# Kernel optimization log

Measured on AMD Instinct MI355X. Metric: run time of the kernel, lower is better.

## Reference

```python
import jax, jax.numpy as jnp
import numpy as np

N, C, T, V = 64, 256, 64, 25

def setup_inputs() -> dict:
    key = jax.random.key(0)
    ks = jax.random.split(key, 11)
    inp = {
        't': jax.random.uniform(ks[0], (1,), dtype=jnp.float32),
        'x': jax.random.normal(ks[1], (N, C, T, V), dtype=jnp.float32),
        'A': jax.random.normal(ks[2], (V, V), dtype=jnp.float32) * 0.2,
    }
    for i in range(4):
        inp[f'w{i+1}'] = jax.random.normal(ks[3 + 2 * i], (C, C), dtype=jnp.float32) * (1.0 / np.sqrt(C))
        inp[f'b{i+1}'] = jax.random.normal(ks[4 + 2 * i], (C,), dtype=jnp.float32) * 0.02
    return inp


def _block(res, A, w, b):
    # graph diffusion over joint dim: A[v,u] @ x[n,c,t,u]
    y = jnp.einsum('vu,nctu->nctv', A, res)
    # 1x1 conv == pointwise channel GEMM
    y = jnp.einsum('oc,nctv->notv', w, y) + b[None, :, None, None]
    return jax.nn.relu(y + res)


def reference(t, x, A, w1, b1, w2, b2, w3, b3, w4, b4):
    # t is unused by the ODE function body (autonomous dynamics)
    res = _block(x, A, w1, b1)
    res = _block(res, A, w2, b2)
    res = _block(res, A, w3, b3)
    res = _block(res, A, w4, b4)
    return res
```

## Files before the change

### kernel.cpp

```cpp
#include <hip/hip_runtime.h>
#include <math.h>

#define NN 64
#define CC 256
#define TT 64
#define VV 25

typedef __bf16 bf16;
typedef __attribute__((ext_vector_type(8)))  __bf16 bf16x8;
typedef __attribute__((ext_vector_type(4)))  __bf16 bf16x4;
typedef __attribute__((ext_vector_type(16))) float  f32x16;

#define RS 40
#define YS 264

#define OFF_SRES  0
#define OFF_SYT   20480
#define OFF_SAB   34208
#define OFF_SBIAS 36256
#define SMEM_BYTES 40352

__global__ void convert_w(const float* __restrict__ w1, const float* __restrict__ w2,
                          const float* __restrict__ w3, const float* __restrict__ w4,
                          bf16* __restrict__ wp) {
    const int gid = blockIdx.x * 256 + threadIdx.x;
    const int e8  = gid * 8;
    const int blk = e8 >> 16;
    const int off = e8 & 65535;
    const int row = off >> 8;
    const int col = off & 255;
    const float* src = (blk == 0) ? w1 : (blk == 1) ? w2 : (blk == 2) ? w3 : w4;
    const float4 f0 = *(const float4*)(src + off);
    const float4 f1 = *(const float4*)(src + off + 4);
    bf16x8 o;
    o[0] = (bf16)f0.x; o[1] = (bf16)f0.y; o[2] = (bf16)f0.z; o[3] = (bf16)f0.w;
    o[4] = (bf16)f1.x; o[5] = (bf16)f1.y; o[6] = (bf16)f1.z; o[7] = (bf16)f1.w;
    const int wv = row >> 6, pair = (row >> 5) & 1, l31 = row & 31;
    const int k = col >> 4, lh = (col >> 3) & 1;
    wp += (((size_t)(blk * 4 + wv) * 16 + k) * 1024) + pair * 512 + (lh * 32 + l31) * 8;
    *(bf16x8*)wp = o;
}

#define MFMA(A, B, C) __builtin_amdgcn_mfma_f32_32x32x16_bf16(A, B, C, 0, 0, 0)

__global__ __launch_bounds__(256, 4) void ode_mfma(
    const float* __restrict__ x, const float* __restrict__ Amat,
    const bf16* __restrict__ wp,
    const float* __restrict__ b1, const float* __restrict__ b2,
    const float* __restrict__ b3, const float* __restrict__ b4,
    float* __restrict__ out)
{
    __shared__ __attribute__((aligned(16))) char smem[SMEM_BYTES];
    bf16*  sres  = (bf16*)(smem + OFF_SRES);
    bf16*  syT   = (bf16*)(smem + OFF_SYT);
    bf16*  sAb   = (bf16*)(smem + OFF_SAB);
    float* sbias = (float*)(smem + OFF_SBIAS);

    const int t    = blockIdx.x;
    const int n    = blockIdx.y;
    const int tid  = threadIdx.x;
    const int wave = tid >> 6;
    const int lane = tid & 63;
    const int lh   = lane >> 5;
    const int l31  = lane & 31;
    const int o0   = wave * 64;

    bf16x8 wA[4], wB[4];
    {
        const bf16* wb0 = wp + ((size_t)wave * 16) * 1024 + lane * 8;
        #pragma unroll
        for (int q = 0; q < 4; ++q) {
            wA[q] = *(const bf16x8*)(wb0 + q * 1024);
            wB[q] = *(const bf16x8*)(wb0 + q * 1024 + 512);
        }
    }

    sbias[0 * CC + tid] = b1[tid];
    sbias[1 * CC + tid] = b2[tid];
    sbias[2 * CC + tid] = b3[tid];
    sbias[3 * CC + tid] = b4[tid];

    for (int i = tid; i < 32 * 32; i += 256) {
        const int v = i >> 5, u = i & 31;
        sAb[i] = (v < VV && u < VV) ? (bf16)Amat[v * VV + u] : (bf16)0.f;
    }

    {
        const float* xb = x + ((size_t)n * CC * TT + t) * VV;
        for (int i = tid; i < CC * VV; i += 256) {
            const int c = i / VV;
            const int v = i - c * VV;
            sres[c * RS + v] = (bf16)xb[(size_t)c * TT * VV + v];
        }
        #pragma unroll
        for (int u = VV; u < 32; ++u) sres[tid * RS + u] = (bf16)0.f;
    }
    __syncthreads();

    const bf16x8 bfA0 = *(const bf16x8*)&sAb[l31 * 32 + lh * 8];
    const bf16x8 bfA1 = *(const bf16x8*)&sAb[l31 * 32 + 16 + lh * 8];

    for (int blk = 0; blk < 4; ++blk) {
        #pragma unroll
        for (int i = 0; i < 2; ++i) {
            const int ct = wave * 2 + i;
            const bf16x8 af0 = *(const bf16x8*)&sres[(ct * 32 + l31) * RS + lh * 8];
            const bf16x8 af1 = *(const bf16x8*)&sres[(ct * 32 + l31) * RS + 16 + lh * 8];
            f32x16 d = {};
            d = MFMA(af0, bfA0, d);
            d = MFMA(af1, bfA1, d);
            if (l31 < VV) {
                #pragma unroll
                for (int g = 0; g < 4; ++g) {
                    bf16x4 p;
                    p[0] = (bf16)d[4 * g];     p[1] = (bf16)d[4 * g + 1];
                    p[2] = (bf16)d[4 * g + 2]; p[3] = (bf16)d[4 * g + 3];
                    *(bf16x4*)&syT[l31 * YS + ct * 32 + 8 * g + 4 * lh] = p;
                }
            }
        }
        __syncthreads();

        const bf16* wbase = wp + ((size_t)(blk * 4 + wave) * 16) * 1024 + lane * 8;

        f32x16 acc0 = {}, acc1 = {};
        bf16x8 yv[4];
        #pragma unroll
        for (int q = 0; q < 4; ++q)
            yv[q] = *(const bf16x8*)&syT[l31 * YS + q * 16 + lh * 8];

        __builtin_amdgcn_s_setprio(1);
        #pragma unroll
        for (int k = 0; k < 16; ++k) {
            const bf16x8 a0 = wA[k & 3];
            const bf16x8 a1 = wB[k & 3];
            const bf16x8 y0 = yv[k & 3];
            if (k < 12) {
                wA[k & 3] = *(const bf16x8*)(wbase + (k + 4) * 1024);
                wB[k & 3] = *(const bf16x8*)(wbase + (k + 4) * 1024 + 512);
                yv[k & 3] = *(const bf16x8*)&syT[l31 * YS + (k + 4) * 16 + lh * 8];
            }
            acc0 = MFMA(a0, y0, acc0);
            acc1 = MFMA(a1, y0, acc1);
        }
        __builtin_amdgcn_s_setprio(0);
        __syncthreads();

        if (blk < 3) {
            const bf16* wn = wp + ((size_t)((blk + 1) * 4 + wave) * 16) * 1024 + lane * 8;
            #pragma unroll
            for (int q = 0; q < 4; ++q) {
                wA[q] = *(const bf16x8*)(wn + q * 1024);
                wB[q] = *(const bf16x8*)(wn + q * 1024 + 512);
            }
        }

        const int v = l31;
        #define EPILOGUE(ACC, OT)                                                   \
            _Pragma("unroll")                                                       \
            for (int g = 0; g < 4; ++g) {                                           \
                const int ob = o0 + (OT) * 32 + 8 * g + 4 * lh;                     \
                const float4 bq = *(const float4*)&sbias[blk * CC + ob];            \
                _Pragma("unroll")                                                   \
                for (int r = 0; r < 4; ++r) {                                       \
                    const int o = ob + r;                                           \
                    float val = ACC[4 * g + r] + ((const float*)&bq)[r]             \
                              + (float)sres[o * RS + v];                            \
                    val = fmaxf(val, 0.f);                                          \
                    if (v < VV) {                                                   \
                        if (blk < 3) sres[o * RS + v] = (bf16)val;                  \
                        else out[(((size_t)n * CC + o) * TT + t) * VV + v] = val;   \
                    }                                                               \
                }                                                                   \
            }
        EPILOGUE(acc0, 0)
        EPILOGUE(acc1, 1)
        #undef EPILOGUE
    }
}

extern "C" void kernel_launch(void* const* d_in, const int* in_sizes, int n_in,
                              void* d_out, int out_size, void* d_ws, size_t ws_size,
                              hipStream_t stream) {
    const float* x  = (const float*)d_in[1];
    const float* A  = (const float*)d_in[2];
    const float* w1 = (const float*)d_in[3];
    const float* b1 = (const float*)d_in[4];
    const float* w2 = (const float*)d_in[5];
    const float* b2 = (const float*)d_in[6];
    const float* w3 = (const float*)d_in[7];
    const float* b3 = (const float*)d_in[8];
    const float* w4 = (const float*)d_in[9];
    const float* b4 = (const float*)d_in[10];
    float* out = (float*)d_out;
    bf16* wp = (bf16*)d_ws;

    convert_w<<<128, 256, 0, stream>>>(w1, w2, w3, w4, wp);
    dim3 grid(TT, NN);
    ode_mfma<<<grid, 256, 0, stream>>>(x, A, wp, b1, b2, b3, b4, out);
}
```

Measured before the change: 334.4 us.

## Fuse graph-diffusion MFMA output directly into channel GEMM via register lane swaps

```diff
diff --git a/kernel.cpp b/kernel.cpp
--- a/kernel.cpp
+++ b/kernel.cpp
@@ -8,17 +8,15 @@
 
 typedef __bf16 bf16;
 typedef __attribute__((ext_vector_type(8)))  __bf16 bf16x8;
-typedef __attribute__((ext_vector_type(4)))  __bf16 bf16x4;
 typedef __attribute__((ext_vector_type(16))) float  f32x16;
+typedef __attribute__((ext_vector_type(4)))  unsigned int uint4v;
 
 #define RS 40
-#define YS 264
 
 #define OFF_SRES  0
-#define OFF_SYT   20480
-#define OFF_SAB   34208
-#define OFF_SBIAS 36256
-#define SMEM_BYTES 40352
+#define OFF_SAB   20480
+#define OFF_SBIAS 22528
+#define SMEM_BYTES 26624
 
 __global__ void convert_w(const float* __restrict__ w1, const float* __restrict__ w2,
                           const float* __restrict__ w3, const float* __restrict__ w4,
@@ -43,6 +41,12 @@
 
 #define MFMA(A, B, C) __builtin_amdgcn_mfma_f32_32x32x16_bf16(A, B, C, 0, 0, 0)
 
+static __device__ __forceinline__ unsigned int pkbf(float a, float b) {
+    unsigned short lo = __builtin_bit_cast(unsigned short, (__bf16)a);
+    unsigned short hi = __builtin_bit_cast(unsigned short, (__bf16)b);
+    return (unsigned int)lo | ((unsigned int)hi << 16);
+}
+
 __global__ __launch_bounds__(256, 4) void ode_mfma(
     const float* __restrict__ x, const float* __restrict__ Amat,
     const bf16* __restrict__ wp,
@@ -52,7 +56,6 @@
 {
     __shared__ __attribute__((aligned(16))) char smem[SMEM_BYTES];
     bf16*  sres  = (bf16*)(smem + OFF_SRES);
-    bf16*  syT   = (bf16*)(smem + OFF_SYT);
     bf16*  sAb   = (bf16*)(smem + OFF_SAB);
     float* sbias = (float*)(smem + OFF_SBIAS);
 
@@ -101,49 +104,49 @@
     const bf16x8 bfA1 = *(const bf16x8*)&sAb[l31 * 32 + 16 + lh * 8];
 
     for (int blk = 0; blk < 4; ++blk) {
+        const bf16* wbase = wp + ((size_t)(blk * 4 + wave) * 16) * 1024 + lane * 8;
+        f32x16 acc0 = {}, acc1 = {};
+
+        bf16x8 afA[2], afB[2];
+        afA[0] = *(const bf16x8*)&sres[l31 * RS + lh * 8];
+        afB[0] = *(const bf16x8*)&sres[l31 * RS + 16 + lh * 8];
+
         #pragma unroll
-        for (int i = 0; i < 2; ++i) {
-            const int ct = wave * 2 + i;
-            const bf16x8 af0 = *(const bf16x8*)&sres[(ct * 32 + l31) * RS + lh * 8];
-            const bf16x8 af1 = *(const bf16x8*)&sres[(ct * 32 + l31) * RS + 16 + lh * 8];
-            f32x16 d = {};
-            d = MFMA(af0, bfA0, d);
-            d = MFMA(af1, bfA1, d);
-            if (l31 < VV) {
-                #pragma unroll
-                for (int g = 0; g < 4; ++g) {
-                    bf16x4 p;
-                    p[0] = (bf16)d[4 * g];     p[1] = (bf16)d[4 * g + 1];
-                    p[2] = (bf16)d[4 * g + 2]; p[3] = (bf16)d[4 * g + 3];
-                    *(bf16x4*)&syT[l31 * YS + ct * 32 + 8 * g + 4 * lh] = p;
-                }
-            }
-        }
-        __syncthreads();
-
-        const bf16* wbase = wp + ((size_t)(blk * 4 + wave) * 16) * 1024 + lane * 8;
-
-        f32x16 acc0 = {}, acc1 = {};
-        bf16x8 yv[4];
-        #pragma unroll
-        for (int q = 0; q < 4; ++q)
-            yv[q] = *(const bf16x8*)&syT[l31 * YS + q * 16 + lh * 8];
-
-        __builtin_amdgcn_s_setprio(1);
-        #pragma unroll
-        for (int k = 0; k < 16; ++k) {
-            const bf16x8 a0 = wA[k & 3];
-            const bf16x8 a1 = wB[k & 3];
-            const bf16x8 y0 = yv[k & 3];
-            if (k < 12) {
-                wA[k & 3] = *(const bf16x8*)(wbase + (k + 4) * 1024);
-                wB[k & 3] = *(const bf16x8*)(wbase + (k + 4) * 1024 + 512);
-                yv[k & 3] = *(const bf16x8*)&syT[l31 * YS + (k + 4) * 16 + lh * 8];
-            }
-            acc0 = MFMA(a0, y0, acc0);
-            acc1 = MFMA(a1, y0, acc1);
-        }
-        __builtin_amdgcn_s_setprio(0);
+        for (int ct = 0; ct < 8; ++ct) {
+            const int cur = ct & 1;
+            if (ct < 7) {
+                afA[cur ^ 1] = *(const bf16x8*)&sres[((ct + 1) * 32 + l31) * RS + lh * 8];
+                afB[cur ^ 1] = *(const bf16x8*)&sres[((ct + 1) * 32 + l31) * RS + 16 + lh * 8];
+            }
+            f32x16 dA = {};
+            dA = MFMA(afA[cur], bfA0, dA);
+            dA = MFMA(afB[cur], bfA1, dA);
+
+            unsigned int w0 = pkbf(dA[0],  dA[1]),  w1 = pkbf(dA[2],  dA[3]);
+            unsigned int w2 = pkbf(dA[4],  dA[5]),  w3 = pkbf(dA[6],  dA[7]);
+            unsigned int w4 = pkbf(dA[8],  dA[9]),  w5 = pkbf(dA[10], dA[11]);
+            unsigned int w6 = pkbf(dA[12], dA[13]), w7 = pkbf(dA[14], dA[15]);
+            asm("v_permlane32_swap_b32 %0, %1" : "+v"(w0), "+v"(w2));
+            asm("v_permlane32_swap_b32 %0, %1" : "+v"(w1), "+v"(w3));
+            asm("v_permlane32_swap_b32 %0, %1" : "+v"(w4), "+v"(w6));
+            asm("v_permlane32_swap_b32 %0, %1" : "+v"(w5), "+v"(w7));
+            const bf16x8 y0 = __builtin_bit_cast(bf16x8, (uint4v){w0, w1, w2, w3});
+            const bf16x8 y1 = __builtin_bit_cast(bf16x8, (uint4v){w4, w5, w6, w7});
+
+            const int k0 = 2 * ct, k1 = 2 * ct + 1;
+            acc0 = MFMA(wA[k0 & 3], y0, acc0);
+            acc1 = MFMA(wB[k0 & 3], y0, acc1);
+            if (k0 + 4 < 16) {
+                wA[k0 & 3] = *(const bf16x8*)(wbase + (k0 + 4) * 1024);
+                wB[k0 & 3] = *(const bf16x8*)(wbase + (k0 + 4) * 1024 + 512);
+            }
+            acc0 = MFMA(wA[k1 & 3], y1, acc0);
+            acc1 = MFMA(wB[k1 & 3], y1, acc1);
+            if (k1 + 4 < 16) {
+                wA[k1 & 3] = *(const bf16x8*)(wbase + (k1 + 4) * 1024);
+                wB[k1 & 3] = *(const bf16x8*)(wbase + (k1 + 4) * 1024 + 512);
+            }
+        }
         __syncthreads();
 
         if (blk < 3) {
@@ -176,6 +179,7 @@
         EPILOGUE(acc0, 0)
         EPILOGUE(acc1, 1)
         #undef EPILOGUE
+        __syncthreads();
     }
 }
 
```

After: 357.3 us. +6.8%, slower.
